# Optimization experiments

Hardware: AMD Instinct MI355X
Metric: run time of the kernel (lower is better)

## Reference

```python
import jax, jax.numpy as jnp
import numpy as np

N_EMBED = 1024
N_HEADS = 16


def setup_inputs() -> dict:
    key = jax.random.key(0)
    k_x, k_wa, k_wp = jax.random.split(key, 3)
    B, T, C = 2, 2048, N_EMBED
    x = jax.random.normal(k_x, (B, T, C), dtype=jnp.float32)
    # flax Dense default: lecun_normal kernel, zero bias; use scaled normal here
    w_attn = jax.random.normal(k_wa, (C, 3 * C), dtype=jnp.float32) / np.sqrt(C)
    b_attn = jnp.zeros((3 * C,), dtype=jnp.float32)
    w_proj = jax.random.normal(k_wp, (C, C), dtype=jnp.float32) / np.sqrt(C)
    b_proj = jnp.zeros((C,), dtype=jnp.float32)
    return {"x": x, "w_attn": w_attn, "b_attn": b_attn,
            "w_proj": w_proj, "b_proj": b_proj}


def reference(x, w_attn, b_attn, w_proj, b_proj):
    B, T, C = x.shape
    H = N_HEADS
    D = C // H
    qkv = x @ w_attn + b_attn                      # [B,T,3C]
    q, k, v = jnp.split(qkv, 3, axis=-1)           # each [B,T,C]
    q = q.reshape(B, T, H, D).swapaxes(1, 2)       # [B,H,T,D]
    k = k.reshape(B, T, H, D).swapaxes(1, 2)
    v = v.reshape(B, T, H, D).swapaxes(1, 2)
    att = jnp.einsum('bhid,bhjd->bhij', q, k) * (1.0 / jnp.sqrt(D))
    causal = jnp.tril(jnp.ones((T, T), dtype=bool))
    att = jnp.where(causal, att, -jnp.inf)
    att = jax.nn.softmax(att, axis=-1)
    y = jnp.einsum('bhij,bhjd->bhid', att, v)      # [B,H,T,D]
    y = y.swapaxes(1, 2).reshape(B, T, C)
    return y @ w_proj + b_proj
```

## Files before the change

### kernel.cpp

```cpp
#include <hip/hip_runtime.h>
#include <hip/hip_bf16.h>

typedef __bf16 bf16x8 __attribute__((ext_vector_type(8)));
typedef float f32x4 __attribute__((ext_vector_type(4)));
typedef float f32x16 __attribute__((ext_vector_type(16)));
typedef unsigned short u16;
typedef unsigned int u32;
typedef u16 u16x8 __attribute__((ext_vector_type(8)));
typedef u32 u32x4 __attribute__((ext_vector_type(4)));

#define SM_SCALE 0.1803368801111244f

#define FEXP2(x) __builtin_amdgcn_exp2f(x)
#define FLOG2(x) __builtin_amdgcn_logf(x)

__device__ inline u16 tobf(float f) {
  u32 u = __builtin_bit_cast(u32, f);
  u32 r = (u + 0x7fffu + ((u >> 16) & 1u)) >> 16;
  return (u16)r;
}

__device__ inline float frombf(u16 h) {
  return __builtin_bit_cast(float, (u32)h << 16);
}

__device__ inline void gload_lds16(const void* g, void* lds) {
  __builtin_amdgcn_global_load_lds(
      (const __attribute__((address_space(1))) u32*)g,
      (__attribute__((address_space(3))) u32*)lds, 16, 0, 0);
}

__device__ __forceinline__ void transpose_body(const float* __restrict__ in,
                                               u16* __restrict__ out, int K,
                                               int N, int bxg, int tid) {
  __shared__ float tile[32][33];
  int nbx = N >> 5;
  int bx = bxg % nbx, by = bxg / nbx;
  int k0 = by << 5, n0 = bx << 5;
  int tx = tid & 31, ty = tid >> 5;
#pragma unroll
  for (int j = 0; j < 4; ++j) {
    int row = ty + j * 8;
    tile[row][tx] = in[(size_t)(k0 + row) * N + n0 + tx];
  }
  __syncthreads();
#pragma unroll
  for (int j = 0; j < 4; ++j) {
    int row = ty + j * 8;
    out[(size_t)(n0 + row) * K + k0 + tx] = tobf(tile[tx][row]);
  }
}

__global__ __launch_bounds__(256) void prep_kernel(
    const float* __restrict__ x, u16* __restrict__ xb,
    const float* __restrict__ wa, u16* __restrict__ wat,
    const float* __restrict__ wp, u16* __restrict__ wpt) {
  const int b = blockIdx.x, tid = threadIdx.x;
  if (b < 2048) {
    int i = b * 256 + tid;
    const float4* p = (const float4*)x + (size_t)i * 2;
    float4 a = p[0], c = p[1];
    u16x8 v;
    v[0] = tobf(a.x); v[1] = tobf(a.y); v[2] = tobf(a.z); v[3] = tobf(a.w);
    v[4] = tobf(c.x); v[5] = tobf(c.y); v[6] = tobf(c.z); v[7] = tobf(c.w);
    *(u16x8*)(xb + (size_t)i * 8) = v;
  } else if (b < 5120) {
    transpose_body(wa, wat, 1024, 3072, b - 2048, tid);
  } else {
    transpose_body(wp, wpt, 1024, 1024, b - 5120, tid);
  }
}

template <int EPI, int BN>
__global__ __launch_bounds__(256) void gemm_bt(
    const u16* __restrict__ A, const u16* __restrict__ Bt,
    const float* __restrict__ bias,
    u16* __restrict__ o0, u16* __restrict__ o1, u16* __restrict__ o2,
    float* __restrict__ fo, int M, int N, int K) {
  constexpr int NF = BN / 32;
  __shared__ __align__(16) u16 As[2][128 * 64];
  __shared__ __align__(16) u16 Bs[2][BN * 64];
  const int tid = threadIdx.x;
  const int lane = tid & 63;
  const int wave = tid >> 6;
  const int nbn = N / BN;
  int bid = (int)blockIdx.x;
  const int cpx = (int)gridDim.x >> 3;
  bid = (bid & 7) * cpx + (bid >> 3);
  const int bm = bid / nbn, bn = bid % nbn;
  const int m0 = bm << 7, n0 = bn * BN;
  const int wr = wave >> 1, wc = wave & 1;
  const int r15 = lane & 15, g = lane >> 4;

  f32x4 acc[4][NF] = {};

#define GSTAGE(buf, kt)                                                    \
  do {                                                                     \
    _Pragma("unroll")                                                      \
    for (int j = 0; j < 4; ++j) {                                          \
      int c = j * 4 + wave;                                                \
      int byte0 = c * 1024 + lane * 16;                                    \
      int row = byte0 >> 7;                                                \
      int colb = (byte0 & 127) ^ ((row & 7) << 4);                         \
      gload_lds16(A + (size_t)(m0 + row) * K + (kt) * 64 + (colb >> 1),    \
                  (char*)As[(buf)] + c * 1024);                            \
    }                                                                      \
    _Pragma("unroll")                                                      \
    for (int j = 0; j < NF; ++j) {                                         \
      int c = j * 4 + wave;                                                \
      int byte0 = c * 1024 + lane * 16;                                    \
      int row = byte0 >> 7;                                                \
      int colb = (byte0 & 127) ^ ((row & 7) << 4);                         \
      gload_lds16(Bt + (size_t)(n0 + row) * K + (kt) * 64 + (colb >> 1),   \
                  (char*)Bs[(buf)] + c * 1024);                            \
    }                                                                      \
  } while (0)

  const int nkt = K >> 6;
  GSTAGE(0, 0);
  asm volatile("s_waitcnt vmcnt(0)");
  __syncthreads();
  for (int kt = 0; kt < nkt; ++kt) {
    const int cur = kt & 1;
    if (kt + 1 < nkt) GSTAGE(cur ^ 1, kt + 1);
#pragma unroll
    for (int kk = 0; kk < 2; ++kk) {
      bf16x8 af[4], bf[NF];
#pragma unroll
      for (int i = 0; i < 4; ++i) {
        int rowA = wr * 64 + i * 16 + r15;
        int ca = (kk * 64 + 16 * g) ^ ((rowA & 7) << 4);
        af[i] = *(const bf16x8*)((const char*)As[cur] + rowA * 128 + ca);
      }
#pragma unroll
      for (int j2 = 0; j2 < NF; ++j2) {
        int rowB = wc * (BN / 2) + j2 * 16 + r15;
        int cb = (kk * 64 + 16 * g) ^ ((rowB & 7) << 4);
        bf[j2] = *(const bf16x8*)((const char*)Bs[cur] + rowB * 128 + cb);
      }
#pragma unroll
      for (int i = 0; i < 4; ++i)
#pragma unroll
        for (int j2 = 0; j2 < NF; ++j2)
          acc[i][j2] = __builtin_amdgcn_mfma_f32_16x16x32_bf16(
              af[i], bf[j2], acc[i][j2], 0, 0, 0);
    }
    asm volatile("s_waitcnt vmcnt(0)");
    __syncthreads();
  }
#undef GSTAGE

#pragma unroll
  for (int j2 = 0; j2 < NF; ++j2) {
    const int n = n0 + wc * (BN / 2) + j2 * 16 + r15;
    const float bv = bias[n];
#pragma unroll
    for (int i = 0; i < 4; ++i) {
      const int mb = m0 + wr * 64 + i * 16 + g * 4;
      float v[4];
#pragma unroll
      for (int rr = 0; rr < 4; ++rr) v[rr] = acc[i][j2][rr] + bv;
      if (EPI == 1) {
#pragma unroll
        for (int rr = 0; rr < 4; ++rr) fo[(size_t)(mb + rr) * N + n] = v[rr];
      } else {
        const int b = mb >> 11, t = mb & 2047;
        const int sec = n >> 10, nn = n & 1023;
        const int h = nn >> 6, d = nn & 63;
        const int bh = b * 16 + h;
        if (sec == 0) {
          u16* base = o0 + ((size_t)bh * 2048 + t) * 64 + d;
#pragma unroll
          for (int rr = 0; rr < 4; ++rr) base[rr * 64] = tobf(v[rr] * SM_SCALE);
        } else if (sec == 1) {
          u16* kb = o1 +
                    (((size_t)(bh * 32 + (t >> 6)) * 4 + (d >> 4)) * 2) * 512 +
                    ((d >> 3) & 1) * 256 + (d & 7);
          const int tb = t & 63;
#pragma unroll
          for (int rr = 0; rr < 4; ++rr) {
            int r = tb + rr;
            kb[(r >> 5) * 512 + (r & 31) * 8] = tobf(v[rr]);
          }
        } else {
          const int tl = t & 63;
          u16* vb = o2 +
                    ((((size_t)(bh * 32 + (t >> 6)) * 4 + (tl >> 4)) * 2 +
                      (d >> 5)) * 512) +
                    ((tl >> 3) & 1) * 256 + (d & 31) * 8 + (tl & 7);
          u32* p = (u32*)vb;
          p[0] = (u32)tobf(v[0]) | ((u32)tobf(v[1]) << 16);
          p[1] = (u32)tobf(v[2]) | ((u32)tobf(v[3]) << 16);
        }
      }
    }
  }
}

static __device__ const signed char PT_C[34] =
    {15,15,15,15,14,14,14,13,13,13,12,12,12,11,11,11,10,10,10,9,9,8,8,7,7,6,6,5,5,4,3,2,1,0};
static __device__ const signed char PT_K0[34] =
    {0,8,16,24,0,10,20,0,9,18,0,8,17,0,8,16,0,7,14,0,10,0,9,0,8,0,7,0,6,0,0,0,0,0};
static __device__ const signed char PT_KN[34] =
    {8,16,24,32,10,20,30,9,18,28,8,17,26,8,16,24,7,14,22,10,20,9,18,8,16,7,14,6,12,10,8,6,4,2};
static __device__ const signed char PT_SL[34] =
    {-1,0,1,2,-1,3,4,-1,5,6,-1,7,8,-1,9,10,-1,11,12,-1,13,-1,14,-1,15,-1,16,-1,17,-2,-2,-2,-2,-2};

__global__ __launch_bounds__(256) void attn_kernel(
    const u16* __restrict__ qb, const u16* __restrict__ kpk,
    const u16* __restrict__ vpk, u16* __restrict__ yb,
    u16* __restrict__ party, float* __restrict__ partM) {
  const int tid = threadIdx.x;
  const int lane = tid & 63;
  const int w = tid >> 6;
  const int q31 = lane & 31, hi = lane >> 5;
  const int bx = blockIdx.x;
  const int pid = bx >> 5, bh = bx & 31;
  const int c = PT_C[pid];
  const int kt0 = PT_K0[pid], ktN = PT_KN[pid];
  const int slot = PT_SL[pid];

  const int q0 = c * 128 + w * 32;
  const int qg = q0 + q31;
  const int qmax = q0 + 31;
  const int ktEnd = min(ktN, (qmax >> 6) + 1);

  const u16* qrow = qb + ((size_t)bh * 2048 + qg) * 64;
  bf16x8 aq[4];
#pragma unroll
  for (int ks = 0; ks < 4; ++ks)
    aq[ks] = *(const bf16x8*)(qrow + ks * 16 + 8 * hi);

  f32x16 o0 = {}, o1 = {};
  float m = -INFINITY, l = 0.f;

  const u16* kbh = kpk + (size_t)bh * 32 * 4096 + lane * 8;
  const u16* vbh = vpk + (size_t)bh * 32 * 4096 + lane * 8;

  for (int kt = kt0; kt < ktEnd; ++kt) {
    const u16* kp = kbh + (size_t)kt * 4096;
    const u16* vp = vbh + (size_t)kt * 4096;

    bf16x8 kf[8];
#pragma unroll
    for (int j = 0; j < 8; ++j) kf[j] = *(const bf16x8*)(kp + j * 512);

    f32x16 s0 = {}, s1 = {};
    __builtin_amdgcn_s_setprio(1);
#pragma unroll
    for (int ks = 0; ks < 4; ++ks) {
      s0 = __builtin_amdgcn_mfma_f32_32x32x16_bf16(kf[2 * ks], aq[ks], s0, 0, 0, 0);
      s1 = __builtin_amdgcn_mfma_f32_32x32x16_bf16(kf[2 * ks + 1], aq[ks], s1, 0, 0, 0);
    }
    __builtin_amdgcn_s_setprio(0);

    if (kt * 64 + 63 > q0) {
      const int thr = qg - kt * 64;
#pragma unroll
      for (int r = 0; r < 16; ++r) {
        const int off = (r & 3) + 8 * (r >> 2) + 4 * hi;
        if (off > thr) s0[r] = -INFINITY;
        if (off + 32 > thr) s1[r] = -INFINITY;
      }
    }
    f32x16 mx;
#pragma unroll
    for (int r = 0; r < 16; ++r) mx[r] = fmaxf(s0[r], s1[r]);
#pragma unroll
    for (int st = 8; st >= 1; st >>= 1)
#pragma unroll
      for (int r = 0; r < st; ++r) mx[r] = fmaxf(mx[r], mx[r + st]);
    float mt = fmaxf(mx[0], __shfl_xor(mx[0], 32, 64));

    if (kt == kt0) {
      m = mt;
    } else if (__any(mt > m + 8.f)) {
      float mnew = fmaxf(m, mt);
      float alpha = FEXP2(m - mnew);
      m = mnew;
      l *= alpha;
#pragma unroll
      for (int r = 0; r < 16; ++r) {
        o0[r] *= alpha;
        o1[r] *= alpha;
      }
    }
#pragma unroll
    for (int r = 0; r < 16; ++r) {
      s0[r] = FEXP2(s0[r] - m);
      s1[r] = FEXP2(s1[r] - m);
    }
    {
      float la = 0.f, lb = 0.f, lc2 = 0.f, ld = 0.f;
#pragma unroll
      for (int r = 0; r < 16; r += 2) {
        la += s0[r];
        lb += s0[r + 1];
        lc2 += s1[r];
        ld += s1[r + 1];
      }
      l += (la + lb) + (lc2 + ld);
    }
    u32 W[16];
#pragma unroll
    for (int i2 = 0; i2 < 8; ++i2) {
      asm("v_cvt_pk_bf16_f32 %0, %1, %2"
          : "=v"(W[i2]) : "v"(s0[2 * i2]), "v"(s0[2 * i2 + 1]));
      asm("v_cvt_pk_bf16_f32 %0, %1, %2"
          : "=v"(W[8 + i2]) : "v"(s1[2 * i2]), "v"(s1[2 * i2 + 1]));
    }
#pragma unroll
    for (int b4 = 0; b4 < 16; b4 += 4) {
      asm("v_permlane32_swap_b32 %0, %1" : "+v"(W[b4]), "+v"(W[b4 + 2]));
      asm("v_permlane32_swap_b32 %0, %1" : "+v"(W[b4 + 1]), "+v"(W[b4 + 3]));
    }
    bf16x8 vf[8];
#pragma unroll
    for (int j = 0; j < 8; ++j) vf[j] = *(const bf16x8*)(vp + j * 512);

    __builtin_amdgcn_s_setprio(1);
#pragma unroll
    for (int ks = 0; ks < 4; ++ks) {
      u32x4 pwv = {W[4 * ks], W[4 * ks + 1], W[4 * ks + 2], W[4 * ks + 3]};
      bf16x8 pf = __builtin_bit_cast(bf16x8, pwv);
      o0 = __builtin_amdgcn_mfma_f32_32x32x16_bf16(vf[2 * ks], pf, o0, 0, 0, 0);
      o1 = __builtin_amdgcn_mfma_f32_32x32x16_bf16(vf[2 * ks + 1], pf, o1, 0, 0, 0);
    }
    __builtin_amdgcn_s_setprio(0);
  }

  l += __shfl_xor(l, 32, 64);
  float inv = 1.0f / l;

  u32* dst;
  if (slot >= 0) {
    dst = (u32*)(party +
                 ((size_t)((slot * 32 + bh) * 128 + w * 32 + q31)) * 64);
  } else {
    int b = bh >> 4, hd = bh & 15;
    dst = (u32*)(yb + ((size_t)b * 2048 + qg) * 1024 + hd * 64);
  }
#pragma unroll
  for (int r = 0; r < 16; r += 2) {
    int d = (r & 3) + 8 * (r >> 2) + 4 * hi;
    dst[d >> 1] = (u32)tobf(o0[r] * inv) | ((u32)tobf(o0[r + 1] * inv) << 16);
    dst[(d + 32) >> 1] =
        (u32)tobf(o1[r] * inv) | ((u32)tobf(o1[r + 1] * inv) << 16);
  }
  if (slot != -2 && hi == 0)
    partM[(pid * 32 + bh) * 128 + w * 32 + q31] = m + FLOG2(l);
}

static __device__ const signed char CB_PID[11] = {0,4,7,10,13,16,19,21,23,25,27};
static __device__ const signed char CB_P[11]   = {4,3,3,3,3,3,2,2,2,2,2};
static __device__ const signed char CB_SL[11]  = {0,3,5,7,9,11,13,14,15,16,17};

__global__ __launch_bounds__(256) void attn_combine(
    const u16* __restrict__ party, const float* __restrict__ partM,
    u16* __restrict__ yb) {
  const int gi = blockIdx.x;
  const int ci = gi >> 5, bh = gi & 31;
  const int c = 15 - ci;
  const int pidb = CB_PID[ci], P = CB_P[ci], slb = CB_SL[ci];
  const int row = threadIdx.x >> 1, off = (threadIdx.x & 1) * 32;

  const float M0 = partM[((pidb + 0) * 32 + bh) * 128 + row];
  const float M1 = partM[((pidb + 1) * 32 + bh) * 128 + row];
  const float M2 = (P > 2) ? partM[((pidb + 2) * 32 + bh) * 128 + row] : -INFINITY;
  const float M3 = (P > 3) ? partM[((pidb + 3) * 32 + bh) * 128 + row] : -INFINITY;
  const float Mm = fmaxf(fmaxf(M0, M1), fmaxf(M2, M3));
  const float w0 = FEXP2(M0 - Mm), w1 = FEXP2(M1 - Mm);
  const float w2 = FEXP2(M2 - Mm), w3 = FEXP2(M3 - Mm);
  const float inv = 1.f / (w0 + w1 + w2 + w3);

  const int b = bh >> 4, head = bh & 15, t = c * 128 + row;
  u16* y = yb + ((size_t)b * 2048 + t) * 1024 + head * 64 + off;

  float acc[32];
#pragma unroll
  for (int j = 0; j < 4; ++j) {
    u16x8 a = *(const u16x8*)(y + j * 8);
#pragma unroll
    for (int e = 0; e < 8; ++e) acc[j * 8 + e] = frombf(a[e]) * w0;
  }
  {
    const u16* p1 = party + ((size_t)((slb + 0) * 32 + bh) * 128 + row) * 64 + off;
#pragma unroll
    for (int j = 0; j < 4; ++j) {
      u16x8 a = *(const u16x8*)(p1 + j * 8);
#pragma unroll
      for (int e = 0; e < 8; ++e) acc[j * 8 + e] += frombf(a[e]) * w1;
    }
  }
  if (P > 2) {
    const u16* p2 = party + ((size_t)((slb + 1) * 32 + bh) * 128 + row) * 64 + off;
#pragma unroll
    for (int j = 0; j < 4; ++j) {
      u16x8 a = *(const u16x8*)(p2 + j * 8);
#pragma unroll
      for (int e = 0; e < 8; ++e) acc[j * 8 + e] += frombf(a[e]) * w2;
    }
  }
  if (P > 3) {
    const u16* p3 = party + ((size_t)((slb + 2) * 32 + bh) * 128 + row) * 64 + off;
#pragma unroll
    for (int j = 0; j < 4; ++j) {
      u16x8 a = *(const u16x8*)(p3 + j * 8);
#pragma unroll
      for (int e = 0; e < 8; ++e) acc[j * 8 + e] += frombf(a[e]) * w3;
    }
  }
#pragma unroll
  for (int j = 0; j < 4; ++j) {
    u16x8 ov;
#pragma unroll
    for (int e = 0; e < 8; ++e) ov[e] = tobf(acc[j * 8 + e] * inv);
    *(u16x8*)(y + j * 8) = ov;
  }
}

extern "C" void kernel_launch(void* const* d_in, const int* in_sizes, int n_in,
                              void* d_out, int out_size, void* d_ws,
                              size_t ws_size, hipStream_t stream) {
  const float* x = (const float*)d_in[0];
  const float* w_attn = (const float*)d_in[1];
  const float* b_attn = (const float*)d_in[2];
  const float* w_proj = (const float*)d_in[3];
  const float* b_proj = (const float*)d_in[4];
  float* out = (float*)d_out;
  char* ws = (char*)d_ws;

  u16* xb = (u16*)ws;
  u16* wat = (u16*)(ws + (8ull << 20));
  u16* wpt = (u16*)(ws + (14ull << 20));
  u16* qbuf = (u16*)(ws + (16ull << 20));
  u16* kpk = (u16*)(ws + (24ull << 20));
  u16* vpk = (u16*)(ws + (32ull << 20));
  u16* yb = (u16*)(ws + (40ull << 20));
  u16* party = (u16*)ws;
  float* partM = (float*)(ws + (10ull << 20));

  prep_kernel<<<6144, 256, 0, stream>>>(x, xb, w_attn, wat, w_proj, wpt);
  gemm_bt<0, 192><<<32 * 16, 256, 0, stream>>>(xb, wat, b_attn, qbuf, kpk,
                                               vpk, nullptr, 4096, 3072, 1024);
  attn_kernel<<<34 * 32, 256, 0, stream>>>(qbuf, kpk, vpk, yb, party, partM);
  attn_combine<<<352, 256, 0, stream>>>(party, partM, yb);
  gemm_bt<1, 64><<<32 * 16, 256, 0, stream>>>(yb, wpt, b_proj, nullptr,
                                              nullptr, nullptr, out, 4096,
                                              1024, 1024);
}
```

Measured before the change: 104.9 us.

## Process 64 query rows per wave to reuse K/V fragments across two tiles

Each wave now handles two 32-row query sub-tiles that share the same K and V fragment loads, doubling MFMA work per global load. The block query tile grows to 256 rows, so the split-K partition tables, partial buffers and combine kernel are rebuilt for 8 query chunks and fewer blocks (640 instead of 1088). This cuts redundant K/V traffic but raises register pressure, may lower occupancy, and gives coarser load balancing across the causal triangle.

```diff
diff --git a/kernel.cpp b/kernel.cpp
--- a/kernel.cpp
+++ b/kernel.cpp
@@ -197,14 +197,14 @@
   }
 }
 
-static __device__ const signed char PT_C[34] =
-    {15,15,15,15,14,14,14,13,13,13,12,12,12,11,11,11,10,10,10,9,9,8,8,7,7,6,6,5,5,4,3,2,1,0};
-static __device__ const signed char PT_K0[34] =
-    {0,8,16,24,0,10,20,0,9,18,0,8,17,0,8,16,0,7,14,0,10,0,9,0,8,0,7,0,6,0,0,0,0,0};
-static __device__ const signed char PT_KN[34] =
-    {8,16,24,32,10,20,30,9,18,28,8,17,26,8,16,24,7,14,22,10,20,9,18,8,16,7,14,6,12,10,8,6,4,2};
-static __device__ const signed char PT_SL[34] =
-    {-1,0,1,2,-1,3,4,-1,5,6,-1,7,8,-1,9,10,-1,11,12,-1,13,-1,14,-1,15,-1,16,-1,17,-2,-2,-2,-2,-2};
+static __device__ const signed char PT_C[20] =
+    {7,7,7,7, 6,6,6,6, 5,5,5, 4,4,4, 3,3, 2,2, 1, 0};
+static __device__ const signed char PT_K0[20] =
+    {0,8,16,24, 0,7,14,21, 0,8,16, 0,7,14, 0,8, 0,6, 0, 0};
+static __device__ const signed char PT_KN[20] =
+    {8,16,24,32, 7,14,21,28, 8,16,24, 7,14,20, 8,16, 6,12, 8, 4};
+static __device__ const signed char PT_SL[20] =
+    {-1,0,1,2, -1,3,4,5, -1,6,7, -1,8,9, -1,10, -1,11, -2, -2};
 
 __global__ __launch_bounds__(256) void attn_kernel(
     const u16* __restrict__ qb, const u16* __restrict__ kpk,
@@ -220,19 +220,22 @@
   const int kt0 = PT_K0[pid], ktN = PT_KN[pid];
   const int slot = PT_SL[pid];
 
-  const int q0 = c * 128 + w * 32;
-  const int qg = q0 + q31;
-  const int qmax = q0 + 31;
-  const int ktEnd = min(ktN, (qmax >> 6) + 1);
-
-  const u16* qrow = qb + ((size_t)bh * 2048 + qg) * 64;
-  bf16x8 aq[4];
-#pragma unroll
-  for (int ks = 0; ks < 4; ++ks)
-    aq[ks] = *(const bf16x8*)(qrow + ks * 16 + 8 * hi);
-
-  f32x16 o0 = {}, o1 = {};
-  float m = -INFINITY, l = 0.f;
+  const int q0 = c * 256 + w * 64;
+  const int qgA = q0 + q31;
+  const int qgB = qgA + 32;
+  const int ktEnd = min(ktN, ((q0 + 63) >> 6) + 1);
+
+  const u16* qrA = qb + ((size_t)bh * 2048 + qgA) * 64;
+  const u16* qrB = qb + ((size_t)bh * 2048 + qgB) * 64;
+  bf16x8 aqA[4], aqB[4];
+#pragma unroll
+  for (int ks = 0; ks < 4; ++ks) {
+    aqA[ks] = *(const bf16x8*)(qrA + ks * 16 + 8 * hi);
+    aqB[ks] = *(const bf16x8*)(qrB + ks * 16 + 8 * hi);
+  }
+
+  f32x16 oA0 = {}, oA1 = {}, oB0 = {}, oB1 = {};
+  float mA = -INFINITY, lA = 0.f, mB = -INFINITY, lB = 0.f;
 
   const u16* kbh = kpk + (size_t)bh * 32 * 4096 + lane * 8;
   const u16* vbh = vpk + (size_t)bh * 32 * 4096 + lane * 8;
@@ -245,74 +248,116 @@
 #pragma unroll
     for (int j = 0; j < 8; ++j) kf[j] = *(const bf16x8*)(kp + j * 512);
 
-    f32x16 s0 = {}, s1 = {};
+    f32x16 sA0 = {}, sA1 = {}, sB0 = {}, sB1 = {};
     __builtin_amdgcn_s_setprio(1);
 #pragma unroll
     for (int ks = 0; ks < 4; ++ks) {
-      s0 = __builtin_amdgcn_mfma_f32_32x32x16_bf16(kf[2 * ks], aq[ks], s0, 0, 0, 0);
-      s1 = __builtin_amdgcn_mfma_f32_32x32x16_bf16(kf[2 * ks + 1], aq[ks], s1, 0, 0, 0);
+      sA0 = __builtin_amdgcn_mfma_f32_32x32x16_bf16(kf[2 * ks], aqA[ks], sA0, 0, 0, 0);
+      sA1 = __builtin_amdgcn_mfma_f32_32x32x16_bf16(kf[2 * ks + 1], aqA[ks], sA1, 0, 0, 0);
+      sB0 = __builtin_amdgcn_mfma_f32_32x32x16_bf16(kf[2 * ks], aqB[ks], sB0, 0, 0, 0);
+      sB1 = __builtin_amdgcn_mfma_f32_32x32x16_bf16(kf[2 * ks + 1], aqB[ks], sB1, 0, 0, 0);
     }
     __builtin_amdgcn_s_setprio(0);
 
     if (kt * 64 + 63 > q0) {
-      const int thr = qg - kt * 64;
+      const int thrA = qgA - kt * 64;
+      const int thrB = thrA + 32;
 #pragma unroll
       for (int r = 0; r < 16; ++r) {
         const int off = (r & 3) + 8 * (r >> 2) + 4 * hi;
-        if (off > thr) s0[r] = -INFINITY;
-        if (off + 32 > thr) s1[r] = -INFINITY;
-      }
-    }
-    f32x16 mx;
-#pragma unroll
-    for (int r = 0; r < 16; ++r) mx[r] = fmaxf(s0[r], s1[r]);
-#pragma unroll
-    for (int st = 8; st >= 1; st >>= 1)
-#pragma unroll
-      for (int r = 0; r < st; ++r) mx[r] = fmaxf(mx[r], mx[r + st]);
-    float mt = fmaxf(mx[0], __shfl_xor(mx[0], 32, 64));
+        if (off > thrA) sA0[r] = -INFINITY;
+        if (off + 32 > thrA) sA1[r] = -INFINITY;
+        if (off > thrB) sB0[r] = -INFINITY;
+        if (off + 32 > thrB) sB1[r] = -INFINITY;
+      }
+    }
+    float pa0 = -INFINITY, pa1 = -INFINITY, pa2 = -INFINITY, pa3 = -INFINITY;
+    float pb0 = -INFINITY, pb1 = -INFINITY, pb2 = -INFINITY, pb3 = -INFINITY;
+#pragma unroll
+    for (int r = 0; r < 16; r += 4) {
+      pa0 = fmaxf(pa0, fmaxf(sA0[r], sA1[r]));
+      pa1 = fmaxf(pa1, fmaxf(sA0[r + 1], sA1[r + 1]));
+      pa2 = fmaxf(pa2, fmaxf(sA0[r + 2], sA1[r + 2]));
+      pa3 = fmaxf(pa3, fmaxf(sA0[r + 3], sA1[r + 3]));
+      pb0 = fmaxf(pb0, fmaxf(sB0[r], sB1[r]));
+      pb1 = fmaxf(pb1, fmaxf(sB0[r + 1], sB1[r + 1]));
+      pb2 = fmaxf(pb2, fmaxf(sB0[r + 2], sB1[r + 2]));
+      pb3 = fmaxf(pb3, fmaxf(sB0[r + 3], sB1[r + 3]));
+    }
+    float mtA = fmaxf(fmaxf(pa0, pa1), fmaxf(pa2, pa3));
+    float mtB = fmaxf(fmaxf(pb0, pb1), fmaxf(pb2, pb3));
+    mtA = fmaxf(mtA, __shfl_xor(mtA, 32, 64));
+    mtB = fmaxf(mtB, __shfl_xor(mtB, 32, 64));
 
     if (kt == kt0) {
-      m = mt;
-    } else if (__any(mt > m + 8.f)) {
-      float mnew = fmaxf(m, mt);
-      float alpha = FEXP2(m - mnew);
-      m = mnew;
-      l *= alpha;
-#pragma unroll
-      for (int r = 0; r < 16; ++r) {
-        o0[r] *= alpha;
-        o1[r] *= alpha;
+      mA = mtA;
+      mB = mtB;
+    } else {
+      if (__any(mtA > mA + 8.f)) {
+        float mnew = fmaxf(mA, mtA);
+        float alpha = FEXP2(mA - mnew);
+        mA = mnew;
+        lA *= alpha;
+#pragma unroll
+        for (int r = 0; r < 16; ++r) {
+          oA0[r] *= alpha;
+          oA1[r] *= alpha;
+        }
+      }
+      if (__any(mtB > mB + 8.f)) {
+        float mnew = fmaxf(mB, mtB);
+        float alpha = FEXP2(mB - mnew);
+        mB = mnew;
+        lB *= alpha;
+#pragma unroll
+        for (int r = 0; r < 16; ++r) {
+          oB0[r] *= alpha;
+          oB1[r] *= alpha;
+        }
       }
     }
 #pragma unroll
     for (int r = 0; r < 16; ++r) {
-      s0[r] = FEXP2(s0[r] - m);
-      s1[r] = FEXP2(s1[r] - m);
+      sA0[r] = FEXP2(sA0[r] - mA);
+      sA1[r] = FEXP2(sA1[r] - mA);
+      sB0[r] = FEXP2(sB0[r] - mB);
+      sB1[r] = FEXP2(sB1[r] - mB);
     }
     {
-      float la = 0.f, lb = 0.f, lc2 = 0.f, ld = 0.f;
+      float a0 = 0.f, a1 = 0.f, a2 = 0.f, a3 = 0.f;
+      float b0 = 0.f, b1 = 0.f, b2 = 0.f, b3 = 0.f;
 #pragma unroll
       for (int r = 0; r < 16; r += 2) {
-        la += s0[r];
-        lb += s0[r + 1];
-        lc2 += s1[r];
-        ld += s1[r + 1];
-      }
-      l += (la + lb) + (lc2 + ld);
-    }
-    u32 W[16];
+        a0 += sA0[r];
+        a1 += sA0[r + 1];
+        a2 += sA1[r];
+        a3 += sA1[r + 1];
+        b0 += sB0[r];
+        b1 += sB0[r + 1];
+        b2 += sB1[r];
+        b3 += sB1[r + 1];
+      }
+      lA += (a0 + a1) + (a2 + a3);
+      lB += (b0 + b1) + (b2 + b3);
+    }
+    u32 WA[16], WB[16];
 #pragma unroll
     for (int i2 = 0; i2 < 8; ++i2) {
       asm("v_cvt_pk_bf16_f32 %0, %1, %2"
-          : "=v"(W[i2]) : "v"(s0[2 * i2]), "v"(s0[2 * i2 + 1]));
+          : "=v"(WA[i2]) : "v"(sA0[2 * i2]), "v"(sA0[2 * i2 + 1]));
       asm("v_cvt_pk_bf16_f32 %0, %1, %2"
-          : "=v"(W[8 + i2]) : "v"(s1[2 * i2]), "v"(s1[2 * i2 + 1]));
+          : "=v"(WA[8 + i2]) : "v"(sA1[2 * i2]), "v"(sA1[2 * i2 + 1]));
+      asm("v_cvt_pk_bf16_f32 %0, %1, %2"
+          : "=v"(WB[i2]) : "v"(sB0[2 * i2]), "v"(sB0[2 * i2 + 1]));
+      asm("v_cvt_pk_bf16_f32 %0, %1, %2"
+          : "=v"(WB[8 + i2]) : "v"(sB1[2 * i2]), "v"(sB1[2 * i2 + 1]));
     }
 #pragma unroll
     for (int b4 = 0; b4 < 16; b4 += 4) {
-      asm("v_permlane32_swap_b32 %0, %1" : "+v"(W[b4]), "+v"(W[b4 + 2]));
-      asm("v_permlane32_swap_b32 %0, %1" : "+v"(W[b4 + 1]), "+v"(W[b4 + 3]));
+      asm("v_permlane32_swap_b32 %0, %1" : "+v"(WA[b4]), "+v"(WA[b4 + 2]));
+      asm("v_permlane32_swap_b32 %0, %1" : "+v"(WA[b4 + 1]), "+v"(WA[b4 + 3]));
+      asm("v_permlane32_swap_b32 %0, %1" : "+v"(WB[b4]), "+v"(WB[b4 + 2]));
+      asm("v_permlane32_swap_b32 %0, %1" : "+v"(WB[b4 + 1]), "+v"(WB[b4 + 3]));
     }
     bf16x8 vf[8];
 #pragma unroll
@@ -321,100 +366,101 @@
     __builtin_amdgcn_s_setprio(1);
 #pragma unroll
     for (int ks = 0; ks < 4; ++ks) {
-      u32x4 pwv = {W[4 * ks], W[4 * ks + 1], W[4 * ks + 2], W[4 * ks + 3]};
-      bf16x8 pf = __builtin_bit_cast(bf16x8, pwv);
-      o0 = __builtin_amdgcn_mfma_f32_32x32x16_bf16(vf[2 * ks], pf, o0, 0, 0, 0);
-      o1 = __builtin_amdgcn_mfma_f32_32x32x16_bf16(vf[2 * ks + 1], pf, o1, 0, 0, 0);
+      u32x4 pa = {WA[4 * ks], WA[4 * ks + 1], WA[4 * ks + 2], WA[4 * ks + 3]};
+      bf16x8 pfA = __builtin_bit_cast(bf16x8, pa);
+      oA0 = __builtin_amdgcn_mfma_f32_32x32x16_bf16(vf[2 * ks], pfA, oA0, 0, 0, 0);
+      oA1 = __builtin_amdgcn_mfma_f32_32x32x16_bf16(vf[2 * ks + 1], pfA, oA1, 0, 0, 0);
+      u32x4 pb = {WB[4 * ks], WB[4 * ks + 1], WB[4 * ks + 2], WB[4 * ks + 3]};
+      bf16x8 pfB = __builtin_bit_cast(bf16x8, pb);
+      oB0 = __builtin_amdgcn_mfma_f32_32x32x16_bf16(vf[2 * ks], pfB, oB0, 0, 0, 0);
+      oB1 = __builtin_amdgcn_mfma_f32_32x32x16_bf16(vf[2 * ks + 1], pfB, oB1, 0, 0, 0);
     }
     __builtin_amdgcn_s_setprio(0);
   }
 
-  l += __shfl_xor(l, 32, 64);
-  float inv = 1.0f / l;
-
-  u32* dst;
+  lA += __shfl_xor(lA, 32, 64);
+  lB += __shfl_xor(lB, 32, 64);
+  const float invA = 1.0f / lA;
+  const float invB = 1.0f / lB;
+
+  u32 *dstA, *dstB;
   if (slot >= 0) {
-    dst = (u32*)(party +
-                 ((size_t)((slot * 32 + bh) * 128 + w * 32 + q31)) * 64);
+    u16* base =
+        party + ((size_t)((slot * 32 + bh) * 256 + w * 64 + q31)) * 64;
+    dstA = (u32*)base;
+    dstB = (u32*)(base + 32 * 64);
   } else {
-    int b = bh >> 4, hd = bh & 15;
-    dst = (u32*)(yb + ((size_t)b * 2048 + qg) * 1024 + hd * 64);
+    const int b = bh >> 4, hd = bh & 15;
+    dstA = (u32*)(yb + ((size_t)b * 2048 + qgA) * 1024 + hd * 64);
+    dstB = (u32*)(yb + ((size_t)b * 2048 + qgB) * 1024 + hd * 64);
   }
 #pragma unroll
   for (int r = 0; r < 16; r += 2) {
-    int d = (r & 3) + 8 * (r >> 2) + 4 * hi;
-    dst[d >> 1] = (u32)tobf(o0[r] * inv) | ((u32)tobf(o0[r + 1] * inv) << 16);
-    dst[(d + 32) >> 1] =
-        (u32)tobf(o1[r] * inv) | ((u32)tobf(o1[r + 1] * inv) << 16);
-  }
-  if (slot != -2 && hi == 0)
-    partM[(pid * 32 + bh) * 128 + w * 32 + q31] = m + FLOG2(l);
-}
-
-static __device__ const signed char CB_PID[11] = {0,4,7,10,13,16,19,21,23,25,27};
-static __device__ const signed char CB_P[11]   = {4,3,3,3,3,3,2,2,2,2,2};
-static __device__ const signed char CB_SL[11]  = {0,3,5,7,9,11,13,14,15,16,17};
+    const int d = (r & 3) + 8 * (r >> 2) + 4 * hi;
+    dstA[d >> 1] = (u32)tobf(oA0[r] * invA) | ((u32)tobf(oA0[r + 1] * invA) << 16);
+    dstA[(d + 32) >> 1] =
+        (u32)tobf(oA1[r] * invA) | ((u32)tobf(oA1[r + 1] * invA) << 16);
+    dstB[d >> 1] = (u32)tobf(oB0[r] * invB) | ((u32)tobf(oB0[r + 1] * invB) << 16);
+    dstB[(d + 32) >> 1] =
+        (u32)tobf(oB1[r] * invB) | ((u32)tobf(oB1[r + 1] * invB) << 16);
+  }
+  if (slot != -2 && hi == 0) {
+    const int ridx = (pid * 32 + bh) * 256 + w * 64 + q31;
+    partM[ridx] = mA + FLOG2(lA);
+    partM[ridx + 32] = mB + FLOG2(lB);
+  }
+}
+
+static __device__ const signed char CB_C[6]   = {7,6,5,4,3,2};
+static __device__ const signed char CB_PID[6] = {0,4,8,11,14,16};
+static __device__ const signed char CB_P[6]   = {4,4,3,3,2,2};
+static __device__ const signed char CB_SL[6]  = {0,3,6,8,10,11};
 
 __global__ __launch_bounds__(256) void attn_combine(
     const u16* __restrict__ party, const float* __restrict__ partM,
     u16* __restrict__ yb) {
   const int gi = blockIdx.x;
   const int ci = gi >> 5, bh = gi & 31;
-  const int c = 15 - ci;
+  const int c = CB_C[ci];
   const int pidb = CB_PID[ci], P = CB_P[ci], slb = CB_SL[ci];
-  const int row = threadIdx.x >> 1, off = (threadIdx.x & 1) * 32;
-
-  const float M0 = partM[((pidb + 0) * 32 + bh) * 128 + row];
-  const float M1 = partM[((pidb + 1) * 32 + bh) * 128 + row];
-  const float M2 = (P > 2) ? partM[((pidb + 2) * 32 + bh) * 128 + row] : -INFINITY;
-  const float M3 = (P > 3) ? partM[((pidb + 3) * 32 + bh) * 128 + row] : -INFINITY;
+  const int row = threadIdx.x;
+
+  const float M0 = partM[((pidb + 0) * 32 + bh) * 256 + row];
+  const float M1 = partM[((pidb + 1) * 32 + bh) * 256 + row];
+  const float M2 = (P > 2) ? partM[((pidb + 2) * 32 + bh) * 256 + row] : -INFINITY;
+  const float M3 = (P > 3) ? partM[((pidb + 3) * 32 + bh) * 256 + row] : -INFINITY;
   const float Mm = fmaxf(fmaxf(M0, M1), fmaxf(M2, M3));
   const float w0 = FEXP2(M0 - Mm), w1 = FEXP2(M1 - Mm);
   const float w2 = FEXP2(M2 - Mm), w3 = FEXP2(M3 - Mm);
   const float inv = 1.f / (w0 + w1 + w2 + w3);
 
-  const int b = bh >> 4, head = bh & 15, t = c * 128 + row;
-  u16* y = yb + ((size_t)b * 2048 + t) * 1024 + head * 64 + off;
-
-  float acc[32];
-#pragma unroll
-  for (int j = 0; j < 4; ++j) {
+  const int b = bh >> 4, head = bh & 15, t = c * 256 + row;
+  u16* y = yb + ((size_t)b * 2048 + t) * 1024 + head * 64;
+  const u16* p1 = party + ((size_t)((slb + 0) * 32 + bh) * 256 + row) * 64;
+  const u16* p2 = party + ((size_t)((slb + 1) * 32 + bh) * 256 + row) * 64;
+  const u16* p3 = party + ((size_t)((slb + 2) * 32 + bh) * 256 + row) * 64;
+
+#pragma unroll
+  for (int j = 0; j < 8; ++j) {
     u16x8 a = *(const u16x8*)(y + j * 8);
-#pragma unroll
-    for (int e = 0; e < 8; ++e) acc[j * 8 + e] = frombf(a[e]) * w0;
-  }
-  {
-    const u16* p1 = party + ((size_t)((slb + 0) * 32 + bh) * 128 + row) * 64 + off;
-#pragma unroll
-    for (int j = 0; j < 4; ++j) {
-      u16x8 a = *(const u16x8*)(p1 + j * 8);
-#pragma unroll
-      for (int e = 0; e < 8; ++e) acc[j * 8 + e] += frombf(a[e]) * w1;
-    }
-  }
-  if (P > 2) {
-    const u16* p2 = party + ((size_t)((slb + 1) * 32 + bh) * 128 + row) * 64 + off;
-#pragma unroll
-    for (int j = 0; j < 4; ++j) {
-      u16x8 a = *(const u16x8*)(p2 + j * 8);
-#pragma unroll
-      for (int e = 0; e < 8; ++e) acc[j * 8 + e] += frombf(a[e]) * w2;
-    }
-  }
-  if (P > 3) {
-    const u16* p3 = party + ((size_t)((slb + 2) * 32 + bh) * 128 + row) * 64 + off;
-#pragma unroll
-    for (int j = 0; j < 4; ++j) {
-      u16x8 a = *(const u16x8*)(p3 + j * 8);
-#pragma unroll
-      for (int e = 0; e < 8; ++e) acc[j * 8 + e] += frombf(a[e]) * w3;
-    }
-  }
-#pragma unroll
-  for (int j = 0; j < 4; ++j) {
+    u16x8 q1 = *(const u16x8*)(p1 + j * 8);
+    float acc[8];
+#pragma unroll
+    for (int e = 0; e < 8; ++e)
+      acc[e] = frombf(a[e]) * w0 + frombf(q1[e]) * w1;
+    if (P > 2) {
+      u16x8 q2 = *(const u16x8*)(p2 + j * 8);
+#pragma unroll
+      for (int e = 0; e < 8; ++e) acc[e] += frombf(q2[e]) * w2;
+    }
+    if (P > 3) {
+      u16x8 q3 = *(const u16x8*)(p3 + j * 8);
+#pragma unroll
+      for (int e = 0; e < 8; ++e) acc[e] += frombf(q3[e]) * w3;
+    }
     u16x8 ov;
 #pragma unroll
-    for (int e = 0; e < 8; ++e) ov[e] = tobf(acc[j * 8 + e] * inv);
+    for (int e = 0; e < 8; ++e) ov[e] = tobf(acc[e] * inv);
     *(u16x8*)(y + j * 8) = ov;
   }
 }
@@ -438,13 +484,13 @@
   u16* vpk = (u16*)(ws + (32ull << 20));
   u16* yb = (u16*)(ws + (40ull << 20));
   u16* party = (u16*)ws;
-  float* partM = (float*)(ws + (10ull << 20));
+  float* partM = (float*)(ws + (13ull << 20));
 
   prep_kernel<<<6144, 256, 0, stream>>>(x, xb, w_attn, wat, w_proj, wpt);
   gemm_bt<0, 192><<<32 * 16, 256, 0, stream>>>(xb, wat, b_attn, qbuf, kpk,
                                                vpk, nullptr, 4096, 3072, 1024);
-  attn_kernel<<<34 * 32, 256, 0, stream>>>(qbuf, kpk, vpk, yb, party, partM);
-  attn_combine<<<352, 256, 0, stream>>>(party, partM, yb);
+  attn_kernel<<<20 * 32, 256, 0, stream>>>(qbuf, kpk, vpk, yb, party, partM);
+  attn_combine<<<192, 256, 0, stream>>>(party, partM, yb);
   gemm_bt<1, 64><<<32 * 16, 256, 0, stream>>>(yb, wpt, b_proj, nullptr,
                                               nullptr, nullptr, out, 4096,
                                               1024, 1024);
```

After: 125.4 us. +19.6%, slower.

## Stage K/V tiles through double-buffered LDS shared across the block's waves

Applied to the files above, without the earlier changes.

Each block now cooperatively copies each 64-key K and V tile from global memory into a double-buffered LDS area using direct global-to-LDS loads, prefetching the next tile while the current one is computed. The four waves read their MFMA operands from LDS instead of each loading the same tile from global or L2. This removes redundant global traffic across waves and hides load latency. In exchange it adds a block-wide barrier and a full vmcnt wait every iteration, and waves whose queries finish earlier keep looping to ktN just to take part in staging.

```diff
diff --git a/kernel.cpp b/kernel.cpp
--- a/kernel.cpp
+++ b/kernel.cpp
@@ -210,6 +210,8 @@
     const u16* __restrict__ qb, const u16* __restrict__ kpk,
     const u16* __restrict__ vpk, u16* __restrict__ yb,
     u16* __restrict__ party, float* __restrict__ partM) {
+  __shared__ __align__(16) u16 Ks[2][4096];
+  __shared__ __align__(16) u16 Vs[2][4096];
   const int tid = threadIdx.x;
   const int lane = tid & 63;
   const int w = tid >> 6;
@@ -223,7 +225,20 @@
   const int q0 = c * 128 + w * 32;
   const int qg = q0 + q31;
   const int qmax = q0 + 31;
-  const int ktEnd = min(ktN, (qmax >> 6) + 1);
+
+  const u16* kbh = kpk + (size_t)bh * 32 * 4096 + lane * 8;
+  const u16* vbh = vpk + (size_t)bh * 32 * 4096 + lane * 8;
+
+#define STAGE(buf, kt)                                                       \
+  do {                                                                       \
+    _Pragma("unroll")                                                        \
+    for (int j = 0; j < 2; ++j) {                                            \
+      gload_lds16(kbh + (size_t)(kt) * 4096 + (w * 2 + j) * 512,             \
+                  (char*)Ks[buf] + (w * 2 + j) * 1024);                      \
+      gload_lds16(vbh + (size_t)(kt) * 4096 + (w * 2 + j) * 512,             \
+                  (char*)Vs[buf] + (w * 2 + j) * 1024);                      \
+    }                                                                        \
+  } while (0)
 
   const u16* qrow = qb + ((size_t)bh * 2048 + qg) * 64;
   bf16x8 aq[4];
@@ -234,100 +249,108 @@
   f32x16 o0 = {}, o1 = {};
   float m = -INFINITY, l = 0.f;
 
-  const u16* kbh = kpk + (size_t)bh * 32 * 4096 + lane * 8;
-  const u16* vbh = vpk + (size_t)bh * 32 * 4096 + lane * 8;
-
-  for (int kt = kt0; kt < ktEnd; ++kt) {
-    const u16* kp = kbh + (size_t)kt * 4096;
-    const u16* vp = vbh + (size_t)kt * 4096;
-
-    bf16x8 kf[8];
-#pragma unroll
-    for (int j = 0; j < 8; ++j) kf[j] = *(const bf16x8*)(kp + j * 512);
-
-    f32x16 s0 = {}, s1 = {};
-    __builtin_amdgcn_s_setprio(1);
-#pragma unroll
-    for (int ks = 0; ks < 4; ++ks) {
-      s0 = __builtin_amdgcn_mfma_f32_32x32x16_bf16(kf[2 * ks], aq[ks], s0, 0, 0, 0);
-      s1 = __builtin_amdgcn_mfma_f32_32x32x16_bf16(kf[2 * ks + 1], aq[ks], s1, 0, 0, 0);
-    }
-    __builtin_amdgcn_s_setprio(0);
-
-    if (kt * 64 + 63 > q0) {
-      const int thr = qg - kt * 64;
+  STAGE(0, kt0);
+  asm volatile("s_waitcnt vmcnt(0)");
+  __syncthreads();
+  int cur = 0;
+  for (int kt = kt0; kt < ktN; ++kt) {
+    if (kt + 1 < ktN) STAGE(cur ^ 1, kt + 1);
+    if (kt * 64 <= qmax) {
+      const char* Kc = (const char*)Ks[cur] + lane * 16;
+      const char* Vc = (const char*)Vs[cur] + lane * 16;
+
+      bf16x8 kf[8];
+#pragma unroll
+      for (int j = 0; j < 8; ++j) kf[j] = *(const bf16x8*)(Kc + j * 1024);
+
+      f32x16 s0 = {}, s1 = {};
+      __builtin_amdgcn_s_setprio(1);
+#pragma unroll
+      for (int ks = 0; ks < 4; ++ks) {
+        s0 = __builtin_amdgcn_mfma_f32_32x32x16_bf16(kf[2 * ks], aq[ks], s0, 0, 0, 0);
+        s1 = __builtin_amdgcn_mfma_f32_32x32x16_bf16(kf[2 * ks + 1], aq[ks], s1, 0, 0, 0);
+      }
+      __builtin_amdgcn_s_setprio(0);
+
+      if (kt * 64 + 63 > q0) {
+        const int thr = qg - kt * 64;
+#pragma unroll
+        for (int r = 0; r < 16; ++r) {
+          const int off = (r & 3) + 8 * (r >> 2) + 4 * hi;
+          if (off > thr) s0[r] = -INFINITY;
+          if (off + 32 > thr) s1[r] = -INFINITY;
+        }
+      }
+      f32x16 mx;
+#pragma unroll
+      for (int r = 0; r < 16; ++r) mx[r] = fmaxf(s0[r], s1[r]);
+#pragma unroll
+      for (int st = 8; st >= 1; st >>= 1)
+#pragma unroll
+        for (int r = 0; r < st; ++r) mx[r] = fmaxf(mx[r], mx[r + st]);
+      float mt = fmaxf(mx[0], __shfl_xor(mx[0], 32, 64));
+
+      if (kt == kt0) {
+        m = mt;
+      } else if (__any(mt > m + 8.f)) {
+        float mnew = fmaxf(m, mt);
+        float alpha = FEXP2(m - mnew);
+        m = mnew;
+        l *= alpha;
+#pragma unroll
+        for (int r = 0; r < 16; ++r) {
+          o0[r] *= alpha;
+          o1[r] *= alpha;
+        }
+      }
 #pragma unroll
       for (int r = 0; r < 16; ++r) {
-        const int off = (r & 3) + 8 * (r >> 2) + 4 * hi;
-        if (off > thr) s0[r] = -INFINITY;
-        if (off + 32 > thr) s1[r] = -INFINITY;
-      }
-    }
-    f32x16 mx;
-#pragma unroll
-    for (int r = 0; r < 16; ++r) mx[r] = fmaxf(s0[r], s1[r]);
-#pragma unroll
-    for (int st = 8; st >= 1; st >>= 1)
-#pragma unroll
-      for (int r = 0; r < st; ++r) mx[r] = fmaxf(mx[r], mx[r + st]);
-    float mt = fmaxf(mx[0], __shfl_xor(mx[0], 32, 64));
-
-    if (kt == kt0) {
-      m = mt;
-    } else if (__any(mt > m + 8.f)) {
-      float mnew = fmaxf(m, mt);
-      float alpha = FEXP2(m - mnew);
-      m = mnew;
-      l *= alpha;
-#pragma unroll
-      for (int r = 0; r < 16; ++r) {
-        o0[r] *= alpha;
-        o1[r] *= alpha;
-      }
-    }
-#pragma unroll
-    for (int r = 0; r < 16; ++r) {
-      s0[r] = FEXP2(s0[r] - m);
-      s1[r] = FEXP2(s1[r] - m);
-    }
-    {
-      float la = 0.f, lb = 0.f, lc2 = 0.f, ld = 0.f;
-#pragma unroll
-      for (int r = 0; r < 16; r += 2) {
-        la += s0[r];
-        lb += s0[r + 1];
-        lc2 += s1[r];
-        ld += s1[r + 1];
-      }
-      l += (la + lb) + (lc2 + ld);
-    }
-    u32 W[16];
-#pragma unroll
-    for (int i2 = 0; i2 < 8; ++i2) {
-      asm("v_cvt_pk_bf16_f32 %0, %1, %2"
-          : "=v"(W[i2]) : "v"(s0[2 * i2]), "v"(s0[2 * i2 + 1]));
-      asm("v_cvt_pk_bf16_f32 %0, %1, %2"
-          : "=v"(W[8 + i2]) : "v"(s1[2 * i2]), "v"(s1[2 * i2 + 1]));
-    }
-#pragma unroll
-    for (int b4 = 0; b4 < 16; b4 += 4) {
-      asm("v_permlane32_swap_b32 %0, %1" : "+v"(W[b4]), "+v"(W[b4 + 2]));
-      asm("v_permlane32_swap_b32 %0, %1" : "+v"(W[b4 + 1]), "+v"(W[b4 + 3]));
-    }
-    bf16x8 vf[8];
-#pragma unroll
-    for (int j = 0; j < 8; ++j) vf[j] = *(const bf16x8*)(vp + j * 512);
-
-    __builtin_amdgcn_s_setprio(1);
-#pragma unroll
-    for (int ks = 0; ks < 4; ++ks) {
-      u32x4 pwv = {W[4 * ks], W[4 * ks + 1], W[4 * ks + 2], W[4 * ks + 3]};
-      bf16x8 pf = __builtin_bit_cast(bf16x8, pwv);
-      o0 = __builtin_amdgcn_mfma_f32_32x32x16_bf16(vf[2 * ks], pf, o0, 0, 0, 0);
-      o1 = __builtin_amdgcn_mfma_f32_32x32x16_bf16(vf[2 * ks + 1], pf, o1, 0, 0, 0);
-    }
-    __builtin_amdgcn_s_setprio(0);
-  }
+        s0[r] = FEXP2(s0[r] - m);
+        s1[r] = FEXP2(s1[r] - m);
+      }
+      {
+        float la = 0.f, lb = 0.f, lc2 = 0.f, ld = 0.f;
+#pragma unroll
+        for (int r = 0; r < 16; r += 2) {
+          la += s0[r];
+          lb += s0[r + 1];
+          lc2 += s1[r];
+          ld += s1[r + 1];
+        }
+        l += (la + lb) + (lc2 + ld);
+      }
+      u32 W[16];
+#pragma unroll
+      for (int i2 = 0; i2 < 8; ++i2) {
+        asm("v_cvt_pk_bf16_f32 %0, %1, %2"
+            : "=v"(W[i2]) : "v"(s0[2 * i2]), "v"(s0[2 * i2 + 1]));
+        asm("v_cvt_pk_bf16_f32 %0, %1, %2"
+            : "=v"(W[8 + i2]) : "v"(s1[2 * i2]), "v"(s1[2 * i2 + 1]));
+      }
+#pragma unroll
+      for (int b4 = 0; b4 < 16; b4 += 4) {
+        asm("v_permlane32_swap_b32 %0, %1" : "+v"(W[b4]), "+v"(W[b4 + 2]));
+        asm("v_permlane32_swap_b32 %0, %1" : "+v"(W[b4 + 1]), "+v"(W[b4 + 3]));
+      }
+      bf16x8 vf[8];
+#pragma unroll
+      for (int j = 0; j < 8; ++j) vf[j] = *(const bf16x8*)(Vc + j * 1024);
+
+      __builtin_amdgcn_s_setprio(1);
+#pragma unroll
+      for (int ks = 0; ks < 4; ++ks) {
+        u32x4 pwv = {W[4 * ks], W[4 * ks + 1], W[4 * ks + 2], W[4 * ks + 3]};
+        bf16x8 pf = __builtin_bit_cast(bf16x8, pwv);
+        o0 = __builtin_amdgcn_mfma_f32_32x32x16_bf16(vf[2 * ks], pf, o0, 0, 0, 0);
+        o1 = __builtin_amdgcn_mfma_f32_32x32x16_bf16(vf[2 * ks + 1], pf, o1, 0, 0, 0);
+      }
+      __builtin_amdgcn_s_setprio(0);
+    }
+    asm volatile("s_waitcnt vmcnt(0)");
+    __syncthreads();
+    cur ^= 1;
+  }
+#undef STAGE
 
   l += __shfl_xor(l, 32, 64);
   float inv = 1.0f / l;
```

Result: slower. 108.9 us (+3.8%).
